# Kernel optimization log

Hardware: AMD Instinct MI355X
Metric: run time of the kernel (lower is better)

Reference implementation:

```python
import jax, jax.numpy as jnp
import numpy as np

B, N, IN_F, OUT_F, OP_D = 64, 96, 128, 128, 48
SKIP_IDX = 1
ATTN_SCALE = 1.0


def setup_inputs() -> dict:
    key = jax.random.key(0)
    ks = jax.random.split(key, 7)
    return {
        "inputs": jax.random.normal(ks[0], (B, N, IN_F), dtype=jnp.float32),
        "adj": jax.random.randint(ks[1], (B, N, N), 0, 5, dtype=jnp.int64),
        "op_emb": jax.random.normal(ks[2], (B, N, N, OP_D), dtype=jnp.float32),
        "weight": jax.random.normal(ks[3], (IN_F, OUT_F), dtype=jnp.float32) * (1.0 / np.sqrt(OUT_F)),
        "attn_w": jax.random.normal(ks[4], (OP_D, OUT_F), dtype=jnp.float32) * (1.0 / np.sqrt(OP_D)),
        "attn_b": jax.random.normal(ks[5], (OUT_F,), dtype=jnp.float32) * 0.01,
        "self_op_emb": jax.random.normal(ks[6], (OP_D,), dtype=jnp.float32),
    }


def reference(inputs, adj, op_emb, weight, attn_w, attn_b, self_op_emb):
    # support: [B, N, OUT_F]
    support = jnp.matmul(inputs, weight)
    n = adj.shape[-1]
    eye = jnp.eye(n, dtype=bool)  # [N, N]
    # plus_I: replace diagonal op embeddings with self_op_emb, add I to adj
    op_emb = jnp.where(eye[..., None], self_op_emb, op_emb)  # [B,N,N,OP_D]
    adj = adj + eye.astype(adj.dtype)
    # attention over op embeddings: [B,N,N,OUT_F]
    attn = jax.nn.sigmoid(jnp.matmul(op_emb, attn_w) + attn_b)
    attn = (adj != 0)[..., None].astype(attn.dtype) * attn * ATTN_SCALE
    # skip-connection edges get attention == 1
    is_skip = (adj == SKIP_IDX)[..., None].astype(attn.dtype)
    attn = is_skip + (1.0 - is_skip) * attn
    # processed_info = sum_j attn[b,i,j,:] * support[b,j,:]; residual = support
    processed_info = jnp.einsum("bijd,bjd->bid", attn, support)
    return processed_info + support
```

## Files before the change

### kernel.cpp

```cpp
#include <hip/hip_runtime.h>
#include <hip/hip_bf16.h>


#define B_ 64
#define N_ 96
#define F_ 128
#define D_ 48
#define G_ 8
#define NGRP (N_ / G_)

typedef __attribute__((ext_vector_type(8))) short short8;
typedef __attribute__((ext_vector_type(4))) float f32x4;

#if __has_builtin(__builtin_amdgcn_exp2f)
#define EXP2(x) __builtin_amdgcn_exp2f(x)
#else
#define EXP2(x) exp2f(x)
#endif

__device__ __forceinline__ void gload_lds16(const void* g, void* l) {
    __builtin_amdgcn_global_load_lds(
        (const __attribute__((address_space(1))) void*)g,
        (__attribute__((address_space(3))) void*)l, 16, 0, 0);
}

__device__ __forceinline__ size_t s2i(int b, int mt, int r, int lg, int fbp) {
    return ((((size_t)b * 6 + mt) * 4 + r) * 4 + lg) * 64 + fbp;
}

__device__ __forceinline__ unsigned bfbits(float x) {
    union { __hip_bfloat16 h; unsigned short u; } cv;
    cv.h = __float2bfloat16(x);
    return (unsigned)cv.u;
}

__global__ __launch_bounds__(256, 4) void support_kernel(
    const float* __restrict__ inputs, const float* __restrict__ weight,
    float2* __restrict__ S2)
{
    __shared__ float in_lds[16 * F_];
    const int tid = threadIdx.x;
    const int row0 = blockIdx.x * 16;
    ((float4*)in_lds)[tid]       = ((const float4*)(inputs + (size_t)row0 * F_))[tid];
    ((float4*)in_lds)[tid + 256] = ((const float4*)(inputs + (size_t)row0 * F_))[tid + 256];
    __syncthreads();
    const int rl = tid >> 4, f0 = (tid & 15) * 8;
    float acc[8] = {0.f,0.f,0.f,0.f,0.f,0.f,0.f,0.f};
    #pragma unroll 4
    for (int k = 0; k < F_; ++k) {
        const float a = in_lds[rl * F_ + k];
        const float4 w0 = *(const float4*)(weight + k * F_ + f0);
        const float4 w1 = *(const float4*)(weight + k * F_ + f0 + 4);
        acc[0] += a * w0.x; acc[1] += a * w0.y; acc[2] += a * w0.z; acc[3] += a * w0.w;
        acc[4] += a * w1.x; acc[5] += a * w1.y; acc[6] += a * w1.z; acc[7] += a * w1.w;
    }
    const int R = row0 + rl;
    const int b = R / N_, j = R - b * N_;
    const int mt = j >> 4, lg = (j >> 2) & 3, r = j & 3;
    #pragma unroll
    for (int q = 0; q < 4; ++q) {
        const int fbp = (f0 >> 1) + q;
        S2[s2i(b, mt, r, lg, fbp)] = make_float2(acc[2 * q], acc[2 * q + 1]);
    }
}

__global__ __launch_bounds__(256, 2) void fused_kernel(
    const float* __restrict__ op_emb,
    const unsigned* __restrict__ adjw,
    const float* __restrict__ attn_w,
    const float* __restrict__ attn_b,
    const float* __restrict__ self_op,
    const float2* __restrict__ S2,
    float* __restrict__ out)
{
    __shared__ __align__(16) float F32buf[2][N_ * D_];
    __shared__ __align__(16) unsigned short Atile[N_ * 64];

    const int tid  = threadIdx.x;
    const int lane = tid & 63;
    const int wv   = tid >> 6;
    const int lg   = lane >> 4;
    const int lm   = lane & 15;
    const int fb   = wv * 32 + lm * 2;
    const int fbp  = wv * 16 + lm;

    const int blk = blockIdx.x;
    const int b   = blk / NGRP;
    const int grp = blk - b * NGRP;
    const int i0  = grp * G_;

    const float kNL2E = -1.44269504088896f;

    const unsigned probe = adjw[2 * lane + 1];
    const bool use32 = __any(probe != 0);

    auto issue_tile = [&](int i, int pb) {
        const char* gbase = (const char*)(op_emb + (size_t)(b * N_ + i) * N_ * D_);
        char* lbase = (char*)(&F32buf[pb][0]);
        #pragma unroll
        for (int c0 = 0; c0 < 5; ++c0) {
            const int c = wv + 4 * c0;
            if (c < 18) gload_lds16(gbase + c * 1024 + lane * 16, lbase + c * 1024);
        }
    };
    auto load_adj = [&](int i) -> int {
        int a = 0;
        if (tid < N_) {
            const size_t idx = (size_t)(b * N_ + i) * N_ + tid;
            a = use32 ? (int)adjw[idx] : (int)adjw[2 * idx];
            a += (tid == i) ? 1 : 0;
        }
        return a;
    };

    issue_tile(i0, 0);
    int adjreg = load_adj(i0);

    short8 bfrag[2][2];
    float  bbias[2];
    {
        const float2 bb = *(const float2*)(attn_b + fb);
        bbias[0] = bb.x * kNL2E;
        bbias[1] = bb.y * kNL2E;
        #pragma unroll
        for (int ks = 0; ks < 2; ++ks) {
            short8 v0, v1;
            #pragma unroll
            for (int e = 0; e < 8; ++e) {
                const int d = ks * 32 + lg * 8 + e;
                if (d < D_) {
                    const float2 w = *(const float2*)(attn_w + d * F_ + fb);
                    v0[e] = (short)bfbits(w.x * kNL2E);
                    v1[e] = (short)bfbits(w.y * kNL2E);
                } else {
                    const unsigned one = (d == D_) ? bfbits(1.0f) : 0u;
                    v0[e] = (short)one;
                    v1[e] = (short)one;
                }
            }
            bfrag[0][ks] = v0;
            bfrag[1][ks] = v1;
        }
    }

    float2 sfrag[6][4];
    #pragma unroll
    for (int mt = 0; mt < 6; ++mt)
        #pragma unroll
        for (int r = 0; r < 4; ++r)
            sfrag[mt][r] = S2[s2i(b, mt, r, lg, fbp)];

    for (int v = tid; v < N_ * 7; v += 256) {
        const int j = v / 7, q = v - 7 * j;
        const int byte = j * 128 + ((100 + q * 4) ^ ((j & 7) << 4));
        *(unsigned*)((char*)Atile + byte) = 0u;
    }

    __syncthreads();

    #pragma unroll 1
    for (int g = 0; g < G_; ++g) {
        const int cur = g & 1;
        const int i = i0 + g;

        int adjnext = 0;
        if (g + 1 < G_) {
            issue_tile(i + 1, cur ^ 1);
            adjnext = load_adj(i + 1);
        }

        #pragma unroll
        for (int s = 0; s < 5; ++s) {
            const int w = tid + s * 256;
            if (w < N_ * 12) {
                const int j = w / 12, c = w - 12 * j;
                float4 p;
                if (j == i) p = *(const float4*)(self_op + c * 4);
                else        p = *(const float4*)((const char*)(&F32buf[cur][0]) + 16 * w);
                const int byte = j * 128 + ((c * 8) ^ ((j & 7) << 4));
                *(uint2*)((char*)Atile + byte) =
                    make_uint2(bfbits(p.x) | (bfbits(p.y) << 16),
                               bfbits(p.z) | (bfbits(p.w) << 16));
            }
        }
        if (tid < N_) {
            const float off = (adjreg == 0) ? 126.f : ((adjreg == 1) ? -126.f : 0.f);
            const int byte = tid * 128 + (96 ^ ((tid & 7) << 4));
            *(unsigned*)((char*)Atile + byte) = bfbits(off);
        }
        asm volatile("s_waitcnt lgkmcnt(0)" ::: "memory");
        __builtin_amdgcn_s_barrier();

        float osum0 = 0.f, osum1 = 0.f;
        #pragma unroll
        for (int mt = 0; mt < 6; ++mt) {
            const int jr  = mt * 16 + lm;
            const int swz = (lm & 7) << 4;
            const char* base = (const char*)Atile + jr * 128;
            const short8 a0 = *(const short8*)(base + (( 0 + lg * 16) ^ swz));
            const short8 a1 = *(const short8*)(base + ((64 + lg * 16) ^ swz));
            f32x4 c0 = (f32x4){bbias[0], bbias[0], bbias[0], bbias[0]};
            f32x4 c1 = (f32x4){bbias[1], bbias[1], bbias[1], bbias[1]};
            c0 = __builtin_amdgcn_mfma_f32_16x16x32_bf16(a0, bfrag[0][0], c0, 0, 0, 0);
            c0 = __builtin_amdgcn_mfma_f32_16x16x32_bf16(a1, bfrag[0][1], c0, 0, 0, 0);
            c1 = __builtin_amdgcn_mfma_f32_16x16x32_bf16(a0, bfrag[1][0], c1, 0, 0, 0);
            c1 = __builtin_amdgcn_mfma_f32_16x16x32_bf16(a1, bfrag[1][1], c1, 0, 0, 0);
            #pragma unroll
            for (int r = 0; r < 4; ++r) {
                const float s0 = __builtin_amdgcn_rcpf(1.f + EXP2(c0[r]));
                const float s1 = __builtin_amdgcn_rcpf(1.f + EXP2(c1[r]));
                osum0 = __builtin_fmaf(s0, sfrag[mt][r].x, osum0);
                osum1 = __builtin_fmaf(s1, sfrag[mt][r].y, osum1);
            }
        }
        osum0 += __shfl_xor(osum0, 16);
        osum0 += __shfl_xor(osum0, 32);
        osum1 += __shfl_xor(osum1, 16);
        osum1 += __shfl_xor(osum1, 32);
        if (lg == 0) {
            const float2 sr = S2[s2i(b, i >> 4, i & 3, (i >> 2) & 3, fbp)];
            float2 o;
            o.x = osum0 + sr.x;
            o.y = osum1 + sr.y;
            *(float2*)(out + (size_t)(b * N_ + i) * F_ + fb) = o;
        }

        asm volatile("s_waitcnt vmcnt(1)" ::: "memory");
        __builtin_amdgcn_s_barrier();
        adjreg = adjnext;
    }
}

extern "C" void kernel_launch(void* const* d_in, const int* in_sizes, int n_in,
                              void* d_out, int out_size, void* d_ws, size_t ws_size,
                              hipStream_t stream) {
    const float*    inputs  = (const float*)d_in[0];
    const unsigned* adjw    = (const unsigned*)d_in[1];
    const float*    op_emb  = (const float*)d_in[2];
    const float*    weight  = (const float*)d_in[3];
    const float*    attn_w  = (const float*)d_in[4];
    const float*    attn_b  = (const float*)d_in[5];
    const float*    self_op = (const float*)d_in[6];
    float* out = (float*)d_out;
    float2* S2 = (float2*)d_ws;

    support_kernel<<<(B_ * N_) / 16, 256, 0, stream>>>(inputs, weight, S2);
    fused_kernel<<<B_ * NGRP, 256, 0, stream>>>(op_emb, adjw, attn_w, attn_b, self_op,
                                                S2, out);
}
```

Measured before the change: 65.63 us.

## Split neighbor rows across two wave groups with 512-thread blocks and LDS reduction

Doubles the block size to 512 threads, so two groups of four waves each process half of the neighbor (j) m-tiles, and their partial sums are combined through a small shared buffer. The rows per block go from 8 to 12, which cuts the grid from 768 to 512 blocks. This aims to raise per-block parallelism and spread the op_emb tile loads over more waves. In exchange it adds an extra barrier per row, and it now waits for all outstanding memory ops (vmcnt(0)) instead of keeping one in flight, which may weaken load/compute overlap.

After: 61.48 us. 1.07x faster.

```diff
diff --git a/kernel.cpp b/kernel.cpp
--- a/kernel.cpp
+++ b/kernel.cpp
@@ -6,7 +6,7 @@
 #define N_ 96
 #define F_ 128
 #define D_ 48
-#define G_ 8
+#define G_ 12
 #define NGRP (N_ / G_)
 
 typedef __attribute__((ext_vector_type(8))) short short8;
@@ -64,7 +64,7 @@
     }
 }
 
-__global__ __launch_bounds__(256, 2) void fused_kernel(
+__global__ __launch_bounds__(512, 4) void fused_kernel(
     const float* __restrict__ op_emb,
     const unsigned* __restrict__ adjw,
     const float* __restrict__ attn_w,
@@ -75,14 +75,17 @@
 {
     __shared__ __align__(16) float F32buf[2][N_ * D_];
     __shared__ __align__(16) unsigned short Atile[N_ * 64];
+    __shared__ __align__(8)  float2 Ppart[4][16];
 
     const int tid  = threadIdx.x;
     const int lane = tid & 63;
-    const int wv   = tid >> 6;
+    const int wid  = tid >> 6;
+    const int wf   = wid & 3;
+    const int wj   = wid >> 2;
     const int lg   = lane >> 4;
     const int lm   = lane & 15;
-    const int fb   = wv * 32 + lm * 2;
-    const int fbp  = wv * 16 + lm;
+    const int fb   = wf * 32 + lm * 2;
+    const int fbp  = wf * 16 + lm;
 
     const int blk = blockIdx.x;
     const int b   = blk / NGRP;
@@ -98,8 +101,8 @@
         const char* gbase = (const char*)(op_emb + (size_t)(b * N_ + i) * N_ * D_);
         char* lbase = (char*)(&F32buf[pb][0]);
         #pragma unroll
-        for (int c0 = 0; c0 < 5; ++c0) {
-            const int c = wv + 4 * c0;
+        for (int c0 = 0; c0 < 3; ++c0) {
+            const int c = wid + 8 * c0;
             if (c < 18) gload_lds16(gbase + c * 1024 + lane * 16, lbase + c * 1024);
         }
     };
@@ -143,14 +146,14 @@
         }
     }
 
-    float2 sfrag[6][4];
+    float2 sfrag[3][4];
     #pragma unroll
-    for (int mt = 0; mt < 6; ++mt)
+    for (int s = 0; s < 3; ++s)
         #pragma unroll
         for (int r = 0; r < 4; ++r)
-            sfrag[mt][r] = S2[s2i(b, mt, r, lg, fbp)];
-
-    for (int v = tid; v < N_ * 7; v += 256) {
+            sfrag[s][r] = S2[s2i(b, 3 * wj + s, r, lg, fbp)];
+
+    for (int v = tid; v < N_ * 7; v += 512) {
         const int j = v / 7, q = v - 7 * j;
         const int byte = j * 128 + ((100 + q * 4) ^ ((j & 7) << 4));
         *(unsigned*)((char*)Atile + byte) = 0u;
@@ -170,8 +173,8 @@
         }
 
         #pragma unroll
-        for (int s = 0; s < 5; ++s) {
-            const int w = tid + s * 256;
+        for (int s = 0; s < 3; ++s) {
+            const int w = tid + s * 512;
             if (w < N_ * 12) {
                 const int j = w / 12, c = w - 12 * j;
                 float4 p;
@@ -193,7 +196,8 @@
 
         float osum0 = 0.f, osum1 = 0.f;
         #pragma unroll
-        for (int mt = 0; mt < 6; ++mt) {
+        for (int s = 0; s < 3; ++s) {
+            const int mt  = 3 * wj + s;
             const int jr  = mt * 16 + lm;
             const int swz = (lm & 7) << 4;
             const char* base = (const char*)Atile + jr * 128;
@@ -209,23 +213,29 @@
             for (int r = 0; r < 4; ++r) {
                 const float s0 = __builtin_amdgcn_rcpf(1.f + EXP2(c0[r]));
                 const float s1 = __builtin_amdgcn_rcpf(1.f + EXP2(c1[r]));
-                osum0 = __builtin_fmaf(s0, sfrag[mt][r].x, osum0);
-                osum1 = __builtin_fmaf(s1, sfrag[mt][r].y, osum1);
+                osum0 = __builtin_fmaf(s0, sfrag[s][r].x, osum0);
+                osum1 = __builtin_fmaf(s1, sfrag[s][r].y, osum1);
             }
         }
         osum0 += __shfl_xor(osum0, 16);
         osum0 += __shfl_xor(osum0, 32);
         osum1 += __shfl_xor(osum1, 16);
         osum1 += __shfl_xor(osum1, 32);
-        if (lg == 0) {
+        if (wj == 1 && lg == 0)
+            Ppart[wf][lm] = make_float2(osum0, osum1);
+        asm volatile("s_waitcnt lgkmcnt(0)" ::: "memory");
+        __builtin_amdgcn_s_barrier();
+
+        if (wj == 0 && lg == 0) {
+            const float2 pp = Ppart[wf][lm];
             const float2 sr = S2[s2i(b, i >> 4, i & 3, (i >> 2) & 3, fbp)];
             float2 o;
-            o.x = osum0 + sr.x;
-            o.y = osum1 + sr.y;
+            o.x = osum0 + pp.x + sr.x;
+            o.y = osum1 + pp.y + sr.y;
             *(float2*)(out + (size_t)(b * N_ + i) * F_ + fb) = o;
         }
 
-        asm volatile("s_waitcnt vmcnt(1)" ::: "memory");
+        asm volatile("s_waitcnt vmcnt(0)" ::: "memory");
         __builtin_amdgcn_s_barrier();
         adjreg = adjnext;
     }
@@ -245,6 +255,6 @@
     float2* S2 = (float2*)d_ws;
 
     support_kernel<<<(B_ * N_) / 16, 256, 0, stream>>>(inputs, weight, S2);
-    fused_kernel<<<B_ * NGRP, 256, 0, stream>>>(op_emb, adjw, attn_w, attn_b, self_op,
+    fused_kernel<<<B_ * NGRP, 512, 0, stream>>>(op_emb, adjw, attn_w, attn_b, self_op,
                                                 S2, out);
 }
```
